# Kernel tuning notes

Hardware: AMD Instinct MI355X
Metric: run time of the kernel (lower is better)

The kernel has to match this reference:

```python
import jax, jax.numpy as jnp
import numpy as np

D_MODEL = 1024
H = 16
D_K = D_MODEL // H


def setup_inputs() -> dict:
    key = jax.random.key(0)
    ks = jax.random.split(key, 7)
    B, S = 4, 2048
    scale = 1.0 / np.sqrt(D_MODEL)
    return {
        "q": jax.random.normal(ks[0], (B, S, D_MODEL), dtype=jnp.float32),
        "k": jax.random.normal(ks[1], (B, S, D_MODEL), dtype=jnp.float32),
        "v": jax.random.normal(ks[2], (B, S, D_MODEL), dtype=jnp.float32),
        "W_q": jax.random.normal(ks[3], (D_MODEL, D_MODEL), dtype=jnp.float32) * scale,
        "W_k": jax.random.normal(ks[4], (D_MODEL, D_MODEL), dtype=jnp.float32) * scale,
        "W_v": jax.random.normal(ks[5], (D_MODEL, D_MODEL), dtype=jnp.float32) * scale,
        "W_o": jax.random.normal(ks[6], (D_MODEL, D_MODEL), dtype=jnp.float32) * scale,
    }


def reference(q, k, v, W_q, W_k, W_v, W_o):
    B, S, _ = q.shape
    # nn.Linear(bias=False): y = x @ W.T
    def proj(x, W):
        return (x @ W.T).reshape(B, -1, H, D_K).transpose(0, 2, 1, 3)  # [B,H,S,d_k]
    Q = proj(q, W_q)
    K = proj(k, W_k)
    V = proj(v, W_v)
    scores = jnp.einsum('bhqd,bhkd->bhqk', Q, K) / jnp.sqrt(jnp.float32(D_K))
    attn = jax.nn.softmax(scores, axis=-1)  # dropout p=0.0 -> identity
    ctx = jnp.einsum('bhqk,bhkd->bhqd', attn, V)
    ctx = ctx.transpose(0, 2, 1, 3).reshape(B, S, H * D_K)
    return ctx @ W_o.T
```

## Files before the change

### kernel.cpp

```cpp
#include <hip/hip_runtime.h>
#include <stdint.h>


typedef __attribute__((ext_vector_type(8))) short bf16x8;
typedef __attribute__((ext_vector_type(4))) float f32x4;

__device__ __forceinline__ void lds_async16(const void* g, void* l) {
  __builtin_amdgcn_global_load_lds(
      (const __attribute__((address_space(1))) void*)g,
      (__attribute__((address_space(3))) void*)l, 16, 0, 0);
}

__device__ __forceinline__ unsigned short f2bf(float f) {
  union { float f; unsigned u; } v; v.f = f;
  unsigned u = v.u + 0x7fffu + ((v.u >> 16) & 1u);
  return (unsigned short)(u >> 16);
}

__device__ __forceinline__ float fast_exp2(float x) {
#if __has_builtin(__builtin_amdgcn_exp2f)
  return __builtin_amdgcn_exp2f(x);
#else
  return exp2f(x);
#endif
}

__device__ __forceinline__ unsigned pk2(float a, float b) {
#if __has_builtin(__builtin_amdgcn_cvt_pk_bf16_f32)
  typedef __bf16 bf16v2 __attribute__((ext_vector_type(2)));
  union { bf16v2 v; unsigned u; } x;
  x.v = __builtin_amdgcn_cvt_pk_bf16_f32(a, b);
  return x.u;
#else
  return (unsigned)f2bf(a) | ((unsigned)f2bf(b) << 16);
#endif
}

__global__ void cvt_kernel(const float* s0, const float* s1, const float* s2, const float* s3,
                           unsigned short* d0, unsigned short* d1, unsigned short* d2, unsigned short* d3,
                           int n4) {
  int which = blockIdx.y;
  const float* s = which == 0 ? s0 : which == 1 ? s1 : which == 2 ? s2 : s3;
  unsigned short* d = which == 0 ? d0 : which == 1 ? d1 : which == 2 ? d2 : d3;
  int i = blockIdx.x * 256 + threadIdx.x;
  if (i < n4) {
    float4 v = ((const float4*)s)[i];
    ushort4 o;
    o.x = f2bf(v.x); o.y = f2bf(v.y); o.z = f2bf(v.z); o.w = f2bf(v.w);
    ((ushort4*)d)[i] = o;
  }
}

struct G256 { f32x4 acc[4][4]; };

__device__ __forceinline__ void stage_half(const unsigned short* __restrict__ src,
                                           int rowbase, int kt, int h,
                                           unsigned short* lds, int tid) {
  const int srow = tid >> 3;
  const int g = tid & 7;
  const int col = ((g ^ (srow & 7)) << 3);
  const unsigned short* s0 = src + (size_t)(rowbase + h * 128 + srow) * 1024 + kt * 64 + col;
  char* d0 = (char*)lds + h * 16384 + tid * 16;
  lds_async16(s0, d0);
  lds_async16(s0 + (size_t)64 * 1024, d0 + 8192);
}

__device__ __forceinline__ void read2(const unsigned short* buf, int rowbase, int c16, int q4,
                                      int tbase, bf16x8 (&fr)[2][2]) {
#pragma unroll
  for (int tt = 0; tt < 2; ++tt)
#pragma unroll
    for (int ks = 0; ks < 2; ++ks) {
      int row = rowbase + (tbase + tt) * 16 + c16;
      fr[tt][ks] = *(const bf16x8*)(buf + row * 64 + (((ks * 4 + q4) ^ (row & 7)) * 8));
    }
}

__device__ __forceinline__ void mfma_quad(G256& G, const bf16x8 (&af)[2][2],
                                          const bf16x8 (&bf)[2][2], int i0, int j0) {
  __builtin_amdgcn_s_setprio(1);
#pragma unroll
  for (int ii = 0; ii < 2; ++ii)
#pragma unroll
    for (int jj = 0; jj < 2; ++jj)
#pragma unroll
      for (int ks = 0; ks < 2; ++ks)
        G.acc[i0 + ii][j0 + jj] = __builtin_amdgcn_mfma_f32_16x16x32_bf16(
            af[ii][ks], bf[jj][ks], G.acc[i0 + ii][j0 + jj], 0, 0, 0);
  __builtin_amdgcn_s_setprio(0);
}

__device__ __forceinline__ void gemm256_core(const unsigned short* __restrict__ A,
                                             const unsigned short* __restrict__ B,
                                             int tm, int tn,
                                             unsigned short* As0, unsigned short* As1,
                                             unsigned short* Bs0, unsigned short* Bs1,
                                             G256& G) {
  const int tid = threadIdx.x;
  const int lane = tid & 63;
  const int wv = tid >> 6;
  const int wm = wv & 1, wn = wv >> 1;
  const int c16 = lane & 15, q4 = lane >> 4;
  const int am = tm * 128, bn = tn * 256;
  const int arow = wm * 64, brow = wn * 64;

#pragma unroll
  for (int i = 0; i < 4; ++i)
#pragma unroll
    for (int j = 0; j < 4; ++j)
#pragma unroll
      for (int r = 0; r < 4; ++r) G.acc[i][j][r] = 0.f;

  stage_half(B, bn, 0, 0, Bs0, tid);
  stage_half(B, bn, 0, 1, Bs0, tid);
  stage_half(A, am, 0, 0, As0, tid);
  stage_half(B, bn, 1, 0, Bs1, tid);
  stage_half(B, bn, 1, 1, Bs1, tid);

  bf16x8 af[2][2], bfa[2][2], bfb[2][2];

  for (int i = 0; i < 8; ++i) {
    const int t1 = 2 * i + 1, t2 = 2 * i + 2, t3 = 2 * i + 3;
    const bool more = (i < 7);
    asm volatile("s_waitcnt vmcnt(4)" ::: "memory");
    __builtin_amdgcn_s_barrier();
    stage_half(A, am, t1, 0, As1, tid);
    read2(As0, arow, c16, q4, 0, af);
    read2(Bs0, brow, c16, q4, 0, bfa);
    mfma_quad(G, af, bfa, 0, 0);
    __builtin_amdgcn_s_barrier();
    read2(Bs0, brow, c16, q4, 2, bfb);
    mfma_quad(G, af, bfb, 0, 2);
    __builtin_amdgcn_s_barrier();
    if (more) stage_half(B, bn, t2, 0, Bs0, tid);
    read2(As0, arow, c16, q4, 2, af);
    mfma_quad(G, af, bfb, 2, 2);
    __builtin_amdgcn_s_barrier();
    if (more) stage_half(B, bn, t2, 1, Bs0, tid);
    mfma_quad(G, af, bfa, 2, 0);
    if (more) { asm volatile("s_waitcnt vmcnt(4)" ::: "memory"); }
    else      { asm volatile("s_waitcnt vmcnt(0)" ::: "memory"); }
    __builtin_amdgcn_s_barrier();
    if (more) stage_half(A, am, t2, 0, As0, tid);
    read2(As1, arow, c16, q4, 0, af);
    read2(Bs1, brow, c16, q4, 0, bfa);
    mfma_quad(G, af, bfa, 0, 0);
    __builtin_amdgcn_s_barrier();
    read2(Bs1, brow, c16, q4, 2, bfb);
    mfma_quad(G, af, bfb, 0, 2);
    __builtin_amdgcn_s_barrier();
    if (more) stage_half(B, bn, t3, 0, Bs1, tid);
    read2(As1, arow, c16, q4, 2, af);
    mfma_quad(G, af, bfb, 2, 2);
    __builtin_amdgcn_s_barrier();
    if (more) stage_half(B, bn, t3, 1, Bs1, tid);
    mfma_quad(G, af, bfa, 2, 0);
  }
}

__global__ __launch_bounds__(512, 1)
void qkv_kernel(const unsigned short* __restrict__ qb, const unsigned short* __restrict__ kb,
                const unsigned short* __restrict__ vb,
                const unsigned short* __restrict__ wq, const unsigned short* __restrict__ wk,
                const unsigned short* __restrict__ wv_,
                unsigned short* __restrict__ Qb, unsigned short* __restrict__ Kb,
                unsigned short* __restrict__ Vtb) {
  __shared__ unsigned short As0[128 * 64];
  __shared__ unsigned short As1[128 * 64];
  __shared__ unsigned short Bs0[256 * 64];
  __shared__ unsigned short Bs1[256 * 64];
  const int z = blockIdx.z;
  const unsigned short* A;
  const unsigned short* B;
  int tm, tn;
  if (z == 0)      { A = qb;  B = wq;  tm = blockIdx.y; tn = blockIdx.x; }
  else if (z == 1) { A = kb;  B = wk;  tm = blockIdx.y; tn = blockIdx.x; }
  else {
    A = wv_; B = vb;
    int idx = blockIdx.y * 4 + blockIdx.x;
    tm = idx >> 5;
    tn = idx & 31;
  }

  G256 G;
  gemm256_core(A, B, tm, tn, As0, As1, Bs0, Bs1, G);

  const int lane = threadIdx.x & 63;
  const int wv = threadIdx.x >> 6;
  const int wm = wv & 1, wn = wv >> 1;
  const int c16 = lane & 15, q4 = lane >> 4;
  const float qscale = 0.125f * 1.44269504f;

#pragma unroll
  for (int i = 0; i < 4; ++i)
#pragma unroll
    for (int j = 0; j < 4; ++j)
#pragma unroll
      for (int r = 0; r < 4; ++r) {
        int m = tm * 128 + wm * 64 + i * 16 + q4 * 4 + r;
        int n = tn * 256 + wn * 64 + j * 16 + c16;
        float val = G.acc[i][j][r];
        if (z < 2) {
          if (z == 0) val *= qscale;
          int b = m >> 11, s_ = m & 2047, h = n >> 6, d = n & 63;
          unsigned short* dst = z == 0 ? Qb : Kb;
          dst[(((size_t)(b * 16 + h) * 2048 + s_) << 6) | d] = f2bf(val);
        } else {
          int h = m >> 6, d = m & 63, b = n >> 11, s_ = n & 2047;
          int sl = s_ & 127;
          int sp = (sl & ~31) | (((sl >> 2) & 3) << 3) | (((sl >> 4) & 1) << 2) | (sl & 3);
          s_ = (s_ & ~127) | sp;
          Vtb[((size_t)((b * 16 + h) * 64 + d) << 11) | s_] = f2bf(val);
        }
      }
}

__global__ __launch_bounds__(512, 1)
void out_gemm(const unsigned short* __restrict__ A, const unsigned short* __restrict__ B,
              float* __restrict__ C) {
  __shared__ unsigned short As0[128 * 64];
  __shared__ unsigned short As1[128 * 64];
  __shared__ unsigned short Bs0[256 * 64];
  __shared__ unsigned short Bs1[256 * 64];
  G256 G;
  gemm256_core(A, B, blockIdx.y, blockIdx.x, As0, As1, Bs0, Bs1, G);
  const int lane = threadIdx.x & 63;
  const int wv = threadIdx.x >> 6;
  const int wm = wv & 1, wn = wv >> 1;
  const int c16 = lane & 15, q4 = lane >> 4;
#pragma unroll
  for (int i = 0; i < 4; ++i)
#pragma unroll
    for (int j = 0; j < 4; ++j)
#pragma unroll
      for (int r = 0; r < 4; ++r) {
        int m = blockIdx.y * 128 + wm * 64 + i * 16 + q4 * 4 + r;
        int n = blockIdx.x * 256 + wn * 64 + j * 16 + c16;
        C[(size_t)m * 1024 + n] = G.acc[i][j][r];
      }
}

__global__ __launch_bounds__(128, 2)
void attn_kernel(const unsigned short* __restrict__ Q,
                 const unsigned short* __restrict__ K,
                 const unsigned short* __restrict__ Vt,
                 unsigned short* __restrict__ ctx) {
  __shared__ unsigned short Ks[2][64 * 64];
  __shared__ unsigned short Vs[2][64 * 64];

  const int tid = threadIdx.x, lane = tid & 63, w = tid >> 6;
  const int c16 = lane & 15, q4 = lane >> 4;
  const int wbase = w * 64;
  const unsigned wgid = blockIdx.x;
  const int bh = (int)((wgid & 7u) * 8 + ((wgid >> 3) & 7u));
  const int qt = (int)(wgid >> 6);
  const unsigned short* Qp = Q + ((size_t)bh * 2048 + qt * 128) * 64;
  const unsigned short* Kp = K + (size_t)bh * 2048 * 64;
  const unsigned short* Vp = Vt + (size_t)bh * 64 * 2048;

  const int srow = tid >> 3;
  const int gcol = (((tid & 7) ^ (srow & 7)) << 3);

  {
    const unsigned short* Qr = Qp + (size_t)srow * 64 + gcol;
    char* base = (char*)Ks + tid * 16;
#pragma unroll
    for (int c = 0; c < 8; ++c) lds_async16(Qr + c * 16 * 64, base + c * 2048);
  }
  __syncthreads();
  const unsigned short* Kflat = &Ks[0][0];
  bf16x8 qf[4][2];
#pragma unroll
  for (int nn = 0; nn < 4; ++nn)
#pragma unroll
    for (int ks = 0; ks < 2; ++ks) {
      int qr = wbase + nn * 16 + c16;
      int pos = (ks * 4 + q4) ^ (qr & 7);
      qf[nn][ks] = *(const bf16x8*)(Kflat + qr * 64 + pos * 8);
    }
  __syncthreads();

  bf16x8 onesf;
  {
    short v = (c16 == 0) ? (short)0x3F80 : (short)0;
#pragma unroll
    for (int j = 0; j < 8; ++j) onesf[j] = v;
  }

  f32x4 oacc[4][4];
  f32x4 lacc[4];
#pragma unroll
  for (int nn = 0; nn < 4; ++nn) {
#pragma unroll
    for (int r = 0; r < 4; ++r) lacc[nn][r] = 0.f;
#pragma unroll
    for (int dj = 0; dj < 4; ++dj)
#pragma unroll
      for (int r = 0; r < 4; ++r) oacc[nn][dj][r] = 0.f;
  }

  const unsigned short* Kr0 = Kp + (size_t)srow * 64 + gcol;
  const unsigned short* Vr0 = Vp + (size_t)srow * 2048 + gcol;

  {
    char* kb = (char*)Ks[0] + tid * 16;
    char* vb = (char*)Vs[0] + tid * 16;
#pragma unroll
    for (int c = 0; c < 4; ++c) {
      lds_async16(Kr0 + (size_t)c * 16 * 64, kb + c * 2048);
      lds_async16(Vr0 + (size_t)c * 16 * 2048, vb + c * 2048);
    }
  }

  int cur = 0;
#pragma unroll 2
  for (int kt = 0; kt < 32; ++kt) {
    __syncthreads();
    if (kt < 31) {
      char* kb = (char*)Ks[cur ^ 1] + tid * 16;
      char* vb = (char*)Vs[cur ^ 1] + tid * 16;
      const unsigned short* Krn = Kr0 + (size_t)(kt + 1) * 64 * 64;
      const unsigned short* Vrn = Vr0 + (size_t)(kt + 1) * 64;
#pragma unroll
      for (int c = 0; c < 4; ++c) {
        lds_async16(Krn + (size_t)c * 16 * 64, kb + c * 2048);
        lds_async16(Vrn + (size_t)c * 16 * 2048, vb + c * 2048);
      }
    }

    const unsigned short* KsC = Ks[cur];
    const unsigned short* VsC = Vs[cur];

    bf16x8 kf[2][2][2];
#pragma unroll
    for (int c = 0; c < 2; ++c)
#pragma unroll
      for (int ms = 0; ms < 2; ++ms) {
        const int row = (c * 2 + ms) * 16 + c16;
        kf[c][ms][0] = *(const bf16x8*)(KsC + row * 64 + ((0 + q4) ^ (row & 7)) * 8);
        kf[c][ms][1] = *(const bf16x8*)(KsC + row * 64 + ((4 + q4) ^ (row & 7)) * 8);
      }
    bf16x8 vf0[4];
#pragma unroll
    for (int dj = 0; dj < 4; ++dj) {
      const int dr = dj * 16 + c16;
      vf0[dj] = *(const bf16x8*)(VsC + dr * 64 + ((q4 ^ (dr & 7))) * 8);
    }

    f32x4 s0[2][4], s1[2][4];
    __builtin_amdgcn_s_setprio(1);
#pragma unroll
    for (int ms = 0; ms < 2; ++ms)
#pragma unroll
      for (int nn = 0; nn < 4; ++nn) {
        f32x4 z = {0.f, 0.f, 0.f, 0.f};
        z = __builtin_amdgcn_mfma_f32_16x16x32_bf16(kf[0][ms][0], qf[nn][0], z, 0, 0, 0);
        z = __builtin_amdgcn_mfma_f32_16x16x32_bf16(kf[0][ms][1], qf[nn][1], z, 0, 0, 0);
        s0[ms][nn] = z;
      }
    __builtin_amdgcn_s_setprio(0);
    bf16x8 vf1[4];
#pragma unroll
    for (int dj = 0; dj < 4; ++dj) {
      const int dr = dj * 16 + c16;
      vf1[dj] = *(const bf16x8*)(VsC + dr * 64 + (((4 + q4) ^ (dr & 7))) * 8);
    }
    __builtin_amdgcn_s_setprio(1);
#pragma unroll
    for (int ms = 0; ms < 2; ++ms)
#pragma unroll
      for (int nn = 0; nn < 4; ++nn) {
        f32x4 z = {0.f, 0.f, 0.f, 0.f};
        z = __builtin_amdgcn_mfma_f32_16x16x32_bf16(kf[1][ms][0], qf[nn][0], z, 0, 0, 0);
        z = __builtin_amdgcn_mfma_f32_16x16x32_bf16(kf[1][ms][1], qf[nn][1], z, 0, 0, 0);
        s1[ms][nn] = z;
      }
    __builtin_amdgcn_s_setprio(0);

    {
      bf16x8 pfv[4];
#pragma unroll
      for (int nn = 0; nn < 4; ++nn) {
        union PU { unsigned u[4]; bf16x8 v; } pf;
        pf.u[0] = pk2(fast_exp2(s0[0][nn][0]), fast_exp2(s0[0][nn][1]));
        pf.u[1] = pk2(fast_exp2(s0[0][nn][2]), fast_exp2(s0[0][nn][3]));
        pf.u[2] = pk2(fast_exp2(s0[1][nn][0]), fast_exp2(s0[1][nn][1]));
        pf.u[3] = pk2(fast_exp2(s0[1][nn][2]), fast_exp2(s0[1][nn][3]));
        pfv[nn] = pf.v;
      }
      __builtin_amdgcn_s_setprio(1);
#pragma unroll
      for (int nn = 0; nn < 4; ++nn)
        lacc[nn] = __builtin_amdgcn_mfma_f32_16x16x32_bf16(pfv[nn], onesf, lacc[nn], 0, 0, 0);
#pragma unroll
      for (int dj = 0; dj < 4; ++dj)
#pragma unroll
        for (int nn = 0; nn < 4; ++nn)
          oacc[nn][dj] = __builtin_amdgcn_mfma_f32_16x16x32_bf16(pfv[nn], vf0[dj], oacc[nn][dj], 0, 0, 0);
      __builtin_amdgcn_s_setprio(0);
    }
    {
      bf16x8 pfv[4];
#pragma unroll
      for (int nn = 0; nn < 4; ++nn) {
        union PU { unsigned u[4]; bf16x8 v; } pf;
        pf.u[0] = pk2(fast_exp2(s1[0][nn][0]), fast_exp2(s1[0][nn][1]));
        pf.u[1] = pk2(fast_exp2(s1[0][nn][2]), fast_exp2(s1[0][nn][3]));
        pf.u[2] = pk2(fast_exp2(s1[1][nn][0]), fast_exp2(s1[1][nn][1]));
        pf.u[3] = pk2(fast_exp2(s1[1][nn][2]), fast_exp2(s1[1][nn][3]));
        pfv[nn] = pf.v;
      }
      __builtin_amdgcn_s_setprio(1);
#pragma unroll
      for (int nn = 0; nn < 4; ++nn)
        lacc[nn] = __builtin_amdgcn_mfma_f32_16x16x32_bf16(pfv[nn], onesf, lacc[nn], 0, 0, 0);
#pragma unroll
      for (int dj = 0; dj < 4; ++dj)
#pragma unroll
        for (int nn = 0; nn < 4; ++nn)
          oacc[nn][dj] = __builtin_amdgcn_mfma_f32_16x16x32_bf16(pfv[nn], vf1[dj], oacc[nn][dj], 0, 0, 0);
      __builtin_amdgcn_s_setprio(0);
    }
    cur ^= 1;
  }

  int b = bh >> 4, h = bh & 15;
#pragma unroll
  for (int nn = 0; nn < 4; ++nn)
#pragma unroll
    for (int r = 0; r < 4; ++r) {
      float l = __shfl(lacc[nn][r], lane & 48, 64);
      float inv = 1.f / l;
      int s_ = qt * 128 + wbase + nn * 16 + q4 * 4 + r;
#pragma unroll
      for (int dj = 0; dj < 4; ++dj) {
        int d = dj * 16 + c16;
        ctx[((size_t)(b * 2048 + s_)) * 1024 + h * 64 + d] = f2bf(oacc[nn][dj][r] * inv);
      }
    }
}

extern "C" void kernel_launch(void* const* d_in, const int* in_sizes, int n_in,
                              void* d_out, int out_size, void* d_ws, size_t ws_size,
                              hipStream_t stream) {
  const float* q  = (const float*)d_in[0];
  const float* k  = (const float*)d_in[1];
  const float* v  = (const float*)d_in[2];
  const float* Wq = (const float*)d_in[3];
  const float* Wk = (const float*)d_in[4];
  const float* Wv = (const float*)d_in[5];
  const float* Wo = (const float*)d_in[6];

  char* ws = (char*)d_ws;
  unsigned short* qb  = (unsigned short*)(ws);
  unsigned short* kb  = (unsigned short*)(ws + (16u << 20));
  unsigned short* vb  = (unsigned short*)(ws + (32u << 20));
  unsigned short* wqb = (unsigned short*)(ws + (48u << 20));
  unsigned short* wkb = (unsigned short*)(ws + (50u << 20));
  unsigned short* wvb = (unsigned short*)(ws + (52u << 20));
  unsigned short* wob = (unsigned short*)(ws + (54u << 20));
  unsigned short* Qb  = (unsigned short*)(ws + (56u << 20));
  unsigned short* Kb  = (unsigned short*)(ws + (72u << 20));
  unsigned short* Vtb = (unsigned short*)(ws + (88u << 20));
  unsigned short* ctxb = qb;

  cvt_kernel<<<dim3(1024, 4), 256, 0, stream>>>(Wq, Wk, Wv, Wo, wqb, wkb, wvb, wob, 262144);
  cvt_kernel<<<dim3(8192, 3), 256, 0, stream>>>(q, k, v, q, qb, kb, vb, qb, 2097152);

  qkv_kernel<<<dim3(4, 64, 3), 512, 0, stream>>>(qb, kb, vb, wqb, wkb, wvb, Qb, Kb, Vtb);

  attn_kernel<<<dim3(1024), 128, 0, stream>>>(Qb, Kb, Vtb, ctxb);

  out_gemm<<<dim3(4, 64), 512, 0, stream>>>(ctxb, wob, (float*)d_out);
}
```

Before: 323.2 us.

## Switch GEMM core from double to triple-buffered LDS pipeline with fewer barriers

Replaces the double-buffered, 8-barrier-per-two-tiles GEMM main loop with a triple-buffered ring where each k-tile prefetches two tiles ahead and uses two barriers per tile. The loop is fully unrolled with modular buffer indices. The aim is to hide global-load latency better and cut barrier stalls in the QKV and output projection GEMMs. In exchange, LDS use grows to 144 KB per block and the vmcnt accounting becomes riskier.

```diff
diff --git a/kernel.cpp b/kernel.cpp
--- a/kernel.cpp
+++ b/kernel.cpp
@@ -93,8 +93,7 @@
 __device__ __forceinline__ void gemm256_core(const unsigned short* __restrict__ A,
                                              const unsigned short* __restrict__ B,
                                              int tm, int tn,
-                                             unsigned short* As0, unsigned short* As1,
-                                             unsigned short* Bs0, unsigned short* Bs1,
+                                             unsigned short* As, unsigned short* Bs,
                                              G256& G) {
   const int tid = threadIdx.x;
   const int lane = tid & 63;
@@ -111,49 +110,37 @@
 #pragma unroll
       for (int r = 0; r < 4; ++r) G.acc[i][j][r] = 0.f;
 
-  stage_half(B, bn, 0, 0, Bs0, tid);
-  stage_half(B, bn, 0, 1, Bs0, tid);
-  stage_half(A, am, 0, 0, As0, tid);
-  stage_half(B, bn, 1, 0, Bs1, tid);
-  stage_half(B, bn, 1, 1, Bs1, tid);
+  stage_half(A, am, 0, 0, As + 0 * 8192, tid);
+  stage_half(B, bn, 0, 0, Bs + 0 * 16384, tid);
+  stage_half(B, bn, 0, 1, Bs + 0 * 16384, tid);
+  stage_half(A, am, 1, 0, As + 1 * 8192, tid);
+  stage_half(B, bn, 1, 0, Bs + 1 * 16384, tid);
+  stage_half(B, bn, 1, 1, Bs + 1 * 16384, tid);
 
   bf16x8 af[2][2], bfa[2][2], bfb[2][2];
 
-  for (int i = 0; i < 8; ++i) {
-    const int t1 = 2 * i + 1, t2 = 2 * i + 2, t3 = 2 * i + 3;
-    const bool more = (i < 7);
-    asm volatile("s_waitcnt vmcnt(4)" ::: "memory");
+#pragma unroll
+  for (int t = 0; t < 16; ++t) {
+    const int bt = t % 3;
+    const int b2 = (t + 2) % 3;
+    const unsigned short* Ab = As + bt * 8192;
+    const unsigned short* Bb = Bs + bt * 16384;
+    if (t < 15) { asm volatile("s_waitcnt vmcnt(6)" ::: "memory"); }
+    else        { asm volatile("s_waitcnt vmcnt(0)" ::: "memory"); }
     __builtin_amdgcn_s_barrier();
-    stage_half(A, am, t1, 0, As1, tid);
-    read2(As0, arow, c16, q4, 0, af);
-    read2(Bs0, brow, c16, q4, 0, bfa);
+    if (t < 14) {
+      stage_half(A, am, t + 2, 0, As + b2 * 8192, tid);
+      stage_half(B, bn, t + 2, 0, Bs + b2 * 16384, tid);
+      stage_half(B, bn, t + 2, 1, Bs + b2 * 16384, tid);
+    }
+    read2(Ab, arow, c16, q4, 0, af);
+    read2(Bb, brow, c16, q4, 0, bfa);
+    read2(Bb, brow, c16, q4, 2, bfb);
     mfma_quad(G, af, bfa, 0, 0);
-    __builtin_amdgcn_s_barrier();
-    read2(Bs0, brow, c16, q4, 2, bfb);
     mfma_quad(G, af, bfb, 0, 2);
     __builtin_amdgcn_s_barrier();
-    if (more) stage_half(B, bn, t2, 0, Bs0, tid);
-    read2(As0, arow, c16, q4, 2, af);
+    read2(Ab, arow, c16, q4, 2, af);
     mfma_quad(G, af, bfb, 2, 2);
-    __builtin_amdgcn_s_barrier();
-    if (more) stage_half(B, bn, t2, 1, Bs0, tid);
-    mfma_quad(G, af, bfa, 2, 0);
-    if (more) { asm volatile("s_waitcnt vmcnt(4)" ::: "memory"); }
-    else      { asm volatile("s_waitcnt vmcnt(0)" ::: "memory"); }
-    __builtin_amdgcn_s_barrier();
-    if (more) stage_half(A, am, t2, 0, As0, tid);
-    read2(As1, arow, c16, q4, 0, af);
-    read2(Bs1, brow, c16, q4, 0, bfa);
-    mfma_quad(G, af, bfa, 0, 0);
-    __builtin_amdgcn_s_barrier();
-    read2(Bs1, brow, c16, q4, 2, bfb);
-    mfma_quad(G, af, bfb, 0, 2);
-    __builtin_amdgcn_s_barrier();
-    if (more) stage_half(B, bn, t3, 0, Bs1, tid);
-    read2(As1, arow, c16, q4, 2, af);
-    mfma_quad(G, af, bfb, 2, 2);
-    __builtin_amdgcn_s_barrier();
-    if (more) stage_half(B, bn, t3, 1, Bs1, tid);
     mfma_quad(G, af, bfa, 2, 0);
   }
 }
@@ -165,10 +152,8 @@
                 const unsigned short* __restrict__ wv_,
                 unsigned short* __restrict__ Qb, unsigned short* __restrict__ Kb,
                 unsigned short* __restrict__ Vtb) {
-  __shared__ unsigned short As0[128 * 64];
-  __shared__ unsigned short As1[128 * 64];
-  __shared__ unsigned short Bs0[256 * 64];
-  __shared__ unsigned short Bs1[256 * 64];
+  __shared__ unsigned short As[3 * 128 * 64];
+  __shared__ unsigned short Bs[3 * 256 * 64];
   const int z = blockIdx.z;
   const unsigned short* A;
   const unsigned short* B;
@@ -183,7 +168,7 @@
   }
 
   G256 G;
-  gemm256_core(A, B, tm, tn, As0, As1, Bs0, Bs1, G);
+  gemm256_core(A, B, tm, tn, As, Bs, G);
 
   const int lane = threadIdx.x & 63;
   const int wv = threadIdx.x >> 6;
@@ -218,12 +203,10 @@
 __global__ __launch_bounds__(512, 1)
 void out_gemm(const unsigned short* __restrict__ A, const unsigned short* __restrict__ B,
               float* __restrict__ C) {
-  __shared__ unsigned short As0[128 * 64];
-  __shared__ unsigned short As1[128 * 64];
-  __shared__ unsigned short Bs0[256 * 64];
-  __shared__ unsigned short Bs1[256 * 64];
+  __shared__ unsigned short As[3 * 128 * 64];
+  __shared__ unsigned short Bs[3 * 256 * 64];
   G256 G;
-  gemm256_core(A, B, blockIdx.y, blockIdx.x, As0, As1, Bs0, Bs1, G);
+  gemm256_core(A, B, blockIdx.y, blockIdx.x, As, Bs, G);
   const int lane = threadIdx.x & 63;
   const int wv = threadIdx.x >> 6;
   const int wm = wv & 1, wn = wv >> 1;
```

New measurement: 322.2 us. Within noise of the previous version (-0.3%).
